# Kernel optimization log

Measured on AMD Instinct MI355X. Metric: run time of the kernel, lower is better.

The kernel has to match this reference:

```python
import jax, jax.numpy as jnp
import numpy as np

B, T, IN, H, OUT, HOR = 512, 720, 6, 128, 3, 360


def _cell(xin, h, c, Wih, Whh, bih, bhh):
    # PyTorch LSTM gate order: i, f, g, o
    g = xin @ Wih.T + h @ Whh.T + bih + bhh
    i, f, gg, o = jnp.split(g, 4, axis=-1)
    c = jax.nn.sigmoid(f) * c + jax.nn.sigmoid(i) * jnp.tanh(gg)
    h = jax.nn.sigmoid(o) * jnp.tanh(c)
    return h, c


def _run_layer(x, Wih, Whh, bih, bhh, reverse):
    xs = x[:, ::-1] if reverse else x
    # hoist input projection out of the scan: (B,T,4H)
    pre = jnp.einsum('bti,gi->btg', xs, Wih) + bih + bhh
    h0 = jnp.zeros((x.shape[0], Whh.shape[1]), x.dtype)

    def step(carry, gt):
        h, c = carry
        g = gt + h @ Whh.T
        i, f, gg, o = jnp.split(g, 4, axis=-1)
        c = jax.nn.sigmoid(f) * c + jax.nn.sigmoid(i) * jnp.tanh(gg)
        h = jax.nn.sigmoid(o) * jnp.tanh(c)
        return (h, c), h

    (hT, cT), ys = jax.lax.scan(step, (h0, h0), jnp.swapaxes(pre, 0, 1))
    ys = jnp.swapaxes(ys, 0, 1)
    if reverse:
        ys = ys[:, ::-1]
    return ys, hT, cT


def reference(x, e0f_Wih, e0f_Whh, e0f_bih, e0f_bhh, e0b_Wih, e0b_Whh, e0b_bih, e0b_bhh,
              e1f_Wih, e1f_Whh, e1f_bih, e1f_bhh, e1b_Wih, e1b_Whh, e1b_bih, e1b_bhh,
              brh_W, brh_b, brc_W, brc_b,
              d0_Wih, d0_Whh, d0_bih, d0_bhh, d1_Wih, d1_Whh, d1_bih, d1_bhh,
              out_W, out_b, start_token):
    b = x.shape[0]
    # bidirectional encoder, layer 0 (input_dim -> H per direction)
    y0f, h0f, c0f = _run_layer(x, e0f_Wih, e0f_Whh, e0f_bih, e0f_bhh, False)
    y0b, h0b, c0b = _run_layer(x, e0b_Wih, e0b_Whh, e0b_bih, e0b_bhh, True)
    y0 = jnp.concatenate([y0f, y0b], axis=-1)  # (B,T,2H)
    # layer 1 (2H -> H per direction); dropout inactive in eval
    _, h1f, c1f = _run_layer(y0, e1f_Wih, e1f_Whh, e1f_bih, e1f_bhh, False)
    _, h1b, c1b = _run_layer(y0, e1b_Wih, e1b_Whh, e1b_bih, e1b_bhh, True)
    # (num_layers, B, 2H): cat fwd/bwd final states per layer
    h_enc = jnp.stack([jnp.concatenate([h0f, h0b], -1), jnp.concatenate([h1f, h1b], -1)])
    c_enc = jnp.stack([jnp.concatenate([c0f, c0b], -1), jnp.concatenate([c1f, c1b], -1)])
    h_dec = h_enc @ brh_W.T + brh_b  # (2,B,H)
    c_dec = c_enc @ brc_W.T + brc_b
    xin0 = jnp.broadcast_to(start_token[0, 0], (b, start_token.shape[-1]))  # (B,3)

    def dec_step(carry, _):
        h0, c0, h1, c1, xin = carry
        h0, c0 = _cell(xin, h0, c0, d0_Wih, d0_Whh, d0_bih, d0_bhh)
        h1, c1 = _cell(h0, h1, c1, d1_Wih, d1_Whh, d1_bih, d1_bhh)
        pred = h1 @ out_W.T + out_b
        return (h0, c0, h1, c1, pred), pred

    carry0 = (h_dec[0], c_dec[0], h_dec[1], c_dec[1], xin0)
    _, preds = jax.lax.scan(dec_step, carry0, None, length=HOR)  # (HOR,B,3)
    return jnp.swapaxes(preds, 0, 1)  # (B,HOR,3)


def setup_inputs() -> dict:
    ks = iter(jax.random.split(jax.random.key(0), 40))

    def p(shape, s=0.05):
        return jax.random.normal(next(ks), shape, dtype=jnp.float32) * s

    d = {"x": jax.random.normal(next(ks), (B, T, IN), dtype=jnp.float32)}
    for name, ind in (("e0f", IN), ("e0b", IN), ("e1f", 2 * H), ("e1b", 2 * H)):
        d[name + "_Wih"] = p((4 * H, ind))
        d[name + "_Whh"] = p((4 * H, H))
        d[name + "_bih"] = p((4 * H,))
        d[name + "_bhh"] = p((4 * H,))
    d["brh_W"] = p((H, 2 * H)); d["brh_b"] = p((H,))
    d["brc_W"] = p((H, 2 * H)); d["brc_b"] = p((H,))
    for name, ind in (("d0", OUT), ("d1", H)):
        d[name + "_Wih"] = p((4 * H, ind))
        d[name + "_Whh"] = p((4 * H, H))
        d[name + "_bih"] = p((4 * H,))
        d[name + "_bhh"] = p((4 * H,))
    d["out_W"] = p((OUT, H)); d["out_b"] = p((OUT,))
    d["start_token"] = p((1, 1, OUT), 0.01)
    return d
```

## Files before the change

kernel.cpp:

```cpp
#include <hip/hip_runtime.h>

typedef __attribute__((ext_vector_type(8))) short bf16x8;
typedef __attribute__((ext_vector_type(4))) float f32x4;

#define MFMA16(a,b,c) __builtin_amdgcn_mfma_f32_16x16x32_bf16((a),(b),(c),0,0,0)

#define T_SEQ  720
#define NB     512
#define HD     128
#define GD     512
#define BT     16
#define HP     136
#define HP0    168
#define YT     256
#define WLP    68
#define HORZ   360

__device__ __forceinline__ float bf2f_(unsigned short u){
  union { unsigned int i; float f; } v; v.i = ((unsigned int)u) << 16; return v.f;
}
__device__ __forceinline__ unsigned short f2bf(float f){
  union { float f; unsigned int i; } v; v.f = f;
  unsigned int r = v.i + 0x7fffu + ((v.i >> 16) & 1u);
  return (unsigned short)(r >> 16);
}
__device__ __forceinline__ float rcp_(float x){ return __builtin_amdgcn_rcpf(x); }
__device__ __forceinline__ float sigm(float x){ return rcp_(1.f + __expf(-x)); }
__device__ __forceinline__ float tanh_(float x){
  float a = fabsf(x);
  float e = __expf(-2.f * a);
  float t = (1.f - e) * rcp_(1.f + e);
  return x >= 0.f ? t : -t;
}
__device__ __forceinline__ bf16x8 cvt8(const float* p){
  bf16x8 r;
  #pragma unroll
  for (int i = 0; i < 8; ++i) r[i] = (short)f2bf(p[i]);
  return r;
}
__device__ __forceinline__ void gl_lds16(const unsigned short* g, unsigned short* l){
  __builtin_amdgcn_global_load_lds(
      (const __attribute__((address_space(1))) void*)(g),
      (__attribute__((address_space(3))) void*)(l), 16, 0, 0);
}

__global__ __launch_bounds__(512, 2)
void enc_layer0_kernel(const float* __restrict__ x,
                       const float* __restrict__ WihF, const float* __restrict__ WhhF,
                       const float* __restrict__ bihF, const float* __restrict__ bhhF,
                       const float* __restrict__ WihB, const float* __restrict__ WhhB,
                       const float* __restrict__ bihB, const float* __restrict__ bhhB,
                       unsigned short* __restrict__ y0,
                       float* __restrict__ ench, float* __restrict__ encc)
{
  __shared__ __align__(16) unsigned short h_buf[2][BT * HP0];
  const int tid  = threadIdx.x;
  const int lane = tid & 63;
  const int w    = tid >> 6;
  const int l15  = lane & 15;
  const int q    = lane >> 4;
  const int dir  = blockIdx.x >> 5;
  const int bbase = (blockIdx.x & 31) * BT;

  const float* Wih = dir ? WihB : WihF;
  const float* Whh = dir ? WhhB : WhhF;
  const float* bih = dir ? bihB : bihF;
  const float* bhh = dir ? bhhB : bhhF;

  bf16x8 bw[4][5];
  float  bias[4];
  #pragma unroll
  for (int g = 0; g < 4; ++g) {
    const int n = g * 128 + w * 16 + l15;
    #pragma unroll
    for (int kt = 0; kt < 4; ++kt)
      bw[g][kt] = cvt8(Whh + n * HD + kt * 32 + q * 8);
    bf16x8 f;
    #pragma unroll
    for (int j = 0; j < 8; ++j) {
      const int kk = q * 8 + j;
      float wv = 0.f;
      if (kk < 6)       wv = Wih[n * 6 + kk];
      else if (kk < 12) wv = Wih[n * 6 + (kk - 6)];
      f[j] = (short)f2bf(wv);
    }
    bw[g][4] = f;
    bias[g] = bih[n] + bhh[n];
  }

  int t = dir ? (T_SEQ - 1) : 0;
  const int dt = dir ? -1 : 1;
  const int xr_ = tid / 6, xk_ = tid % 6;

  float cst[4] = {0.f, 0.f, 0.f, 0.f};
  for (int i = tid; i < 2 * BT * HP0; i += 512) (&h_buf[0][0])[i] = 0;
  __syncthreads();
  float xv_cur = 0.f;
  if (tid < 96) {
    const float v0 = x[((size_t)(bbase + xr_) * T_SEQ + t) * 6 + xk_];
    const unsigned short hi = f2bf(v0);
    h_buf[0][xr_ * HP0 + 128 + xk_] = hi;
    h_buf[0][xr_ * HP0 + 134 + xk_] = f2bf(v0 - bf2f_(hi));
    xv_cur = x[((size_t)(bbase + xr_) * T_SEQ + t + dt) * 6 + xk_];
  }
  __syncthreads();

  for (int s = 0; s < T_SEQ; ++s, t += dt) {
    const int cur = s & 1, nxt = cur ^ 1;

    if (s > 0 && tid < 256) {
      const int b = tid >> 4, c8 = tid & 15;
      const bf16x8 hv = *reinterpret_cast<const bf16x8*>(&h_buf[cur][b * HP0 + c8 * 8]);
      *reinterpret_cast<bf16x8*>(y0 + ((size_t)(bbase + b) * T_SEQ + (t - dt)) * 256 + dir * HD + c8 * 8) = hv;
    }
    float xv_next = 0.f;
    if (tid < 96 && s + 2 < T_SEQ)
      xv_next = x[((size_t)(bbase + xr_) * T_SEQ + (t + 2 * dt)) * 6 + xk_];

    f32x4 acc[4];
    #pragma unroll
    for (int g = 0; g < 4; ++g) {
      acc[g][0] = bias[g]; acc[g][1] = bias[g];
      acc[g][2] = bias[g]; acc[g][3] = bias[g];
    }
    #pragma unroll
    for (int kt = 0; kt < 5; ++kt) {
      const bf16x8 af = *reinterpret_cast<const bf16x8*>(&h_buf[cur][l15 * HP0 + kt * 32 + q * 8]);
      #pragma unroll
      for (int g = 0; g < 4; ++g) acc[g] = MFMA16(af, bw[g][kt], acc[g]);
    }

    #pragma unroll
    for (int r = 0; r < 4; ++r) {
      const float i_ = acc[0][r], f_ = acc[1][r], g_ = acc[2][r], o_ = acc[3][r];
      const float c_ = sigm(f_) * cst[r] + sigm(i_) * tanh_(g_);
      cst[r] = c_;
      const float h_ = sigm(o_) * tanh_(c_);
      h_buf[nxt][(q * 4 + r) * HP0 + w * 16 + l15] = f2bf(h_);
      if (s == T_SEQ - 1) {
        const int b   = bbase + q * 4 + r;
        const int cix = w * 16 + l15;
        ench[(dir * NB + b) * HD + cix] = h_;
        encc[(dir * NB + b) * HD + cix] = c_;
      }
    }
    if (tid < 96 && s + 1 < T_SEQ) {
      const unsigned short hi = f2bf(xv_cur);
      h_buf[nxt][xr_ * HP0 + 128 + xk_] = hi;
      h_buf[nxt][xr_ * HP0 + 134 + xk_] = f2bf(xv_cur - bf2f_(hi));
    }
    xv_cur = xv_next;
    __syncthreads();
  }
  if (tid < 256) {
    const int cur = T_SEQ & 1;
    const int b = tid >> 4, c8 = tid & 15;
    const bf16x8 hv = *reinterpret_cast<const bf16x8*>(&h_buf[cur][b * HP0 + c8 * 8]);
    const int tl = dir ? 0 : (T_SEQ - 1);
    *reinterpret_cast<bf16x8*>(y0 + ((size_t)(bbase + b) * T_SEQ + tl) * 256 + dir * HD + c8 * 8) = hv;
  }
}

__global__ __launch_bounds__(512, 2)
void enc_layer1_kernel(const unsigned short* __restrict__ y0,
                       const float* __restrict__ WihF, const float* __restrict__ WhhF,
                       const float* __restrict__ bihF, const float* __restrict__ bhhF,
                       const float* __restrict__ WihB, const float* __restrict__ WhhB,
                       const float* __restrict__ bihB, const float* __restrict__ bhhB,
                       float* __restrict__ ench, float* __restrict__ encc)
{
  __shared__ __align__(16) unsigned short wlds[GD * WLP];
  __shared__ __align__(16) unsigned short ybuf[2][BT * YT];
  __shared__ __align__(16) unsigned short h_buf[2][BT * HP];

  const int tid  = threadIdx.x;
  const int lane = tid & 63;
  const int w    = tid >> 6;
  const int l15  = lane & 15;
  const int q    = lane >> 4;
  const int dir  = blockIdx.x >> 5;
  const int bbase = (blockIdx.x & 31) * BT;

  const float* Wih = dir ? WihB : WihF;
  const float* Whh = dir ? WhhB : WhhF;
  const float* bih = dir ? bihB : bihF;
  const float* bhh = dir ? bhhB : bhhF;

  for (int i = tid; i < GD * 8; i += 512) {
    const int n = i >> 3, c8 = i & 7;
    *reinterpret_cast<bf16x8*>(&wlds[n * WLP + c8 * 8]) = cvt8(Wih + n * 256 + c8 * 8);
  }

  bf16x8 bw[4][10];
  float  bias[4];
  int    nofs[4];
  #pragma unroll
  for (int g = 0; g < 4; ++g) {
    const int n = g * 128 + w * 16 + l15;
    nofs[g] = n * WLP;
    #pragma unroll
    for (int kt = 2; kt < 8; ++kt)  bw[g][kt - 2] = cvt8(Wih + n * 256 + kt * 32 + q * 8);
    #pragma unroll
    for (int kt = 8; kt < 12; ++kt) bw[g][kt - 2] = cvt8(Whh + n * HD + (kt - 8) * 32 + q * 8);
    bias[g] = bih[n] + bhh[n];
  }

  const int sb   = 2 * w + (lane >> 5);
  const int cimg = lane & 31;
  const int sig  = (cimg & 16) | ((cimg & 15) ^ (sb & 15));
  const size_t grow = (size_t)(bbase + sb) * T_SEQ * 256 + (size_t)sig * 8;
  unsigned short* ldst0 = &ybuf[0][w * 512];
  unsigned short* ldst1 = &ybuf[1][w * 512];

  int t = dir ? (T_SEQ - 1) : 0;
  const int dt = dir ? -1 : 1;

  float cst[4] = {0.f, 0.f, 0.f, 0.f};
  for (int i = tid; i < 2 * BT * HP; i += 512) (&h_buf[0][0])[i] = 0;
  gl_lds16(y0 + grow + (size_t)t * 256, ldst0);
  __syncthreads();

  for (int s = 0; s < T_SEQ; ++s, t += dt) {
    const int cur = s & 1, nxt = cur ^ 1;

    if (s + 1 < T_SEQ)
      gl_lds16(y0 + grow + (size_t)(t + dt) * 256, cur ? ldst0 : ldst1);

    f32x4 acc[4];
    #pragma unroll
    for (int g = 0; g < 4; ++g) {
      acc[g][0] = bias[g]; acc[g][1] = bias[g];
      acc[g][2] = bias[g]; acc[g][3] = bias[g];
    }
    #pragma unroll
    for (int kt = 0; kt < 2; ++kt) {
      const int swz = ((kt * 4 + q) & 15) ^ l15;
      const bf16x8 af = *reinterpret_cast<const bf16x8*>(&ybuf[cur][l15 * YT + swz * 8]);
      #pragma unroll
      for (int g = 0; g < 4; ++g) {
        const bf16x8 bl = *reinterpret_cast<const bf16x8*>(&wlds[nofs[g] + kt * 32 + q * 8]);
        acc[g] = MFMA16(af, bl, acc[g]);
      }
    }
    #pragma unroll
    for (int kt = 2; kt < 8; ++kt) {
      const int c   = kt * 4 + q;
      const int swz = (c & 16) | ((c & 15) ^ l15);
      const bf16x8 af = *reinterpret_cast<const bf16x8*>(&ybuf[cur][l15 * YT + swz * 8]);
      #pragma unroll
      for (int g = 0; g < 4; ++g) acc[g] = MFMA16(af, bw[g][kt - 2], acc[g]);
    }
    #pragma unroll
    for (int kt = 8; kt < 12; ++kt) {
      const bf16x8 af = *reinterpret_cast<const bf16x8*>(&h_buf[cur][l15 * HP + (kt - 8) * 32 + q * 8]);
      #pragma unroll
      for (int g = 0; g < 4; ++g) acc[g] = MFMA16(af, bw[g][kt - 2], acc[g]);
    }

    #pragma unroll
    for (int r = 0; r < 4; ++r) {
      const float i_ = acc[0][r], f_ = acc[1][r], g_ = acc[2][r], o_ = acc[3][r];
      const float c_ = sigm(f_) * cst[r] + sigm(i_) * tanh_(g_);
      cst[r] = c_;
      const float h_ = sigm(o_) * tanh_(c_);
      h_buf[nxt][(q * 4 + r) * HP + w * 16 + l15] = f2bf(h_);
      if (s == T_SEQ - 1) {
        const int b   = bbase + q * 4 + r;
        const int cix = w * 16 + l15;
        ench[(dir * NB + b) * HD + cix] = h_;
        encc[(dir * NB + b) * HD + cix] = c_;
      }
    }
    __syncthreads();
  }
}

__global__ void bridge_kernel(const float* __restrict__ ench0, const float* __restrict__ encc0,
                              const float* __restrict__ ench1, const float* __restrict__ encc1,
                              const float* __restrict__ brhW, const float* __restrict__ brhb,
                              const float* __restrict__ brcW, const float* __restrict__ brcb,
                              float* __restrict__ dech, float* __restrict__ decc)
{
  const int idx = blockIdx.x * 256 + threadIdx.x;
  const int sel = idx >> 17;
  const int l   = (idx >> 16) & 1;
  const int b   = (idx >> 7) & 511;
  const int j   = idx & 127;
  const float* W  = sel ? brcW : brhW;
  const float* bb = sel ? brcb : brhb;
  const float* s0 = sel ? (l ? encc1 : encc0) : (l ? ench1 : ench0);
  float a = bb[j];
  for (int k = 0; k < 128; ++k) a += W[j * 256 + k] * s0[b * 128 + k];
  for (int k = 0; k < 128; ++k) a += W[j * 256 + 128 + k] * s0[(512 + b) * 128 + k];
  float* dst = sel ? decc : dech;
  dst[(l * 512 + b) * 128 + j] = a;
}

__global__ __launch_bounds__(512, 2)
void decoder_kernel(const float* __restrict__ dech, const float* __restrict__ decc,
                    const float* __restrict__ W0ih, const float* __restrict__ W0hh,
                    const float* __restrict__ b0ih, const float* __restrict__ b0hh,
                    const float* __restrict__ W1ih, const float* __restrict__ W1hh,
                    const float* __restrict__ b1ih, const float* __restrict__ b1hh,
                    const float* __restrict__ outW, const float* __restrict__ outb,
                    const float* __restrict__ stok,
                    float* __restrict__ out)
{
  __shared__ __align__(16) unsigned short w0lds[GD * WLP];
  __shared__ __align__(16) unsigned short w1lds[GD * WLP];
  __shared__ __align__(16) unsigned short h0_buf[2][BT * HP];
  __shared__ __align__(16) unsigned short h1_buf[2][BT * HP];

  const int tid  = threadIdx.x;
  const int lane = tid & 63;
  const int w    = tid >> 6;
  const int l15  = lane & 15;
  const int q    = lane >> 4;
  const int bbase = blockIdx.x * BT;

  for (int i = tid; i < GD * 8; i += 512) {
    const int n = i >> 3, c8 = i & 7;
    *reinterpret_cast<bf16x8*>(&w0lds[n * WLP + c8 * 8]) = cvt8(W0hh + n * HD + c8 * 8);
    *reinterpret_cast<bf16x8*>(&w1lds[n * WLP + c8 * 8]) = cvt8(W1ih + n * HD + c8 * 8);
  }

  bf16x8 bw0[4][2];
  bf16x8 bw1[4][6];
  float  xw0[4][3], bias0[4], bias1[4];
  int    nofs[4];
  #pragma unroll
  for (int g = 0; g < 4; ++g) {
    const int n = g * 128 + w * 16 + l15;
    nofs[g] = n * WLP;
    #pragma unroll
    for (int kt = 2; kt < 4; ++kt) {
      bw0[g][kt - 2] = cvt8(W0hh + n * HD + kt * 32 + q * 8);
      bw1[g][kt - 2] = cvt8(W1ih + n * HD + kt * 32 + q * 8);
    }
    #pragma unroll
    for (int kt = 4; kt < 8; ++kt)
      bw1[g][kt - 2] = cvt8(W1hh + n * HD + (kt - 4) * 32 + q * 8);
    #pragma unroll
    for (int k = 0; k < 3; ++k) xw0[g][k] = W0ih[n * 3 + k];
    bias0[g] = b0ih[n] + b0hh[n];
    bias1[g] = b1ih[n] + b1hh[n];
  }

  bf16x8 owf[4];
  float outb_s = 0.f;
  {
    bf16x8 z;
    #pragma unroll
    for (int i = 0; i < 8; ++i) z[i] = 0;
    #pragma unroll
    for (int kt = 0; kt < 4; ++kt) owf[kt] = z;
    if (l15 < 3) {
      #pragma unroll
      for (int kt = 0; kt < 4; ++kt) owf[kt] = cvt8(outW + l15 * HD + kt * 32 + q * 8);
      outb_s = outb[l15];
    }
  }

  float c0[4], c1[4];
  #pragma unroll
  for (int r = 0; r < 4; ++r) {
    const int b   = bbase + q * 4 + r;
    const int cix = w * 16 + l15;
    c0[r] = decc[b * HD + cix];
    c1[r] = decc[(NB + b) * HD + cix];
  }
  for (int i = tid; i < BT * HD; i += 512) {
    const int b = i >> 7, cix = i & 127;
    h0_buf[0][b * HP + cix] = f2bf(dech[(bbase + b) * HD + cix]);
    h1_buf[0][b * HP + cix] = f2bf(dech[(NB + bbase + b) * HD + cix]);
  }
  float xr[4][3];
  {
    const float s0 = stok[0], s1 = stok[1], s2 = stok[2];
    #pragma unroll
    for (int r = 0; r < 4; ++r) { xr[r][0] = s0; xr[r][1] = s1; xr[r][2] = s2; }
  }
  __syncthreads();

  for (int s = 0; s < HORZ; ++s) {
    const int cur = s & 1, nxt = cur ^ 1;

    f32x4 acc[4];
    #pragma unroll
    for (int g = 0; g < 4; ++g)
      #pragma unroll
      for (int r = 0; r < 4; ++r)
        acc[g][r] = bias0[g] + xw0[g][0] * xr[r][0] + xw0[g][1] * xr[r][1] + xw0[g][2] * xr[r][2];
    #pragma unroll
    for (int kt = 0; kt < 2; ++kt) {
      const bf16x8 af = *reinterpret_cast<const bf16x8*>(&h0_buf[cur][l15 * HP + kt * 32 + q * 8]);
      #pragma unroll
      for (int g = 0; g < 4; ++g) {
        const bf16x8 bl = *reinterpret_cast<const bf16x8*>(&w0lds[nofs[g] + kt * 32 + q * 8]);
        acc[g] = MFMA16(af, bl, acc[g]);
      }
    }
    #pragma unroll
    for (int kt = 2; kt < 4; ++kt) {
      const bf16x8 af = *reinterpret_cast<const bf16x8*>(&h0_buf[cur][l15 * HP + kt * 32 + q * 8]);
      #pragma unroll
      for (int g = 0; g < 4; ++g) acc[g] = MFMA16(af, bw0[g][kt - 2], acc[g]);
    }
    #pragma unroll
    for (int r = 0; r < 4; ++r) {
      const float i_ = acc[0][r], f_ = acc[1][r], g_ = acc[2][r], o_ = acc[3][r];
      const float c_ = sigm(f_) * c0[r] + sigm(i_) * tanh_(g_);
      c0[r] = c_;
      const float h_ = sigm(o_) * tanh_(c_);
      h0_buf[nxt][(q * 4 + r) * HP + w * 16 + l15] = f2bf(h_);
    }
    __syncthreads();

    #pragma unroll
    for (int g = 0; g < 4; ++g) {
      acc[g][0] = bias1[g]; acc[g][1] = bias1[g];
      acc[g][2] = bias1[g]; acc[g][3] = bias1[g];
    }
    #pragma unroll
    for (int kt = 0; kt < 2; ++kt) {
      const bf16x8 af = *reinterpret_cast<const bf16x8*>(&h0_buf[nxt][l15 * HP + kt * 32 + q * 8]);
      #pragma unroll
      for (int g = 0; g < 4; ++g) {
        const bf16x8 bl = *reinterpret_cast<const bf16x8*>(&w1lds[nofs[g] + kt * 32 + q * 8]);
        acc[g] = MFMA16(af, bl, acc[g]);
      }
    }
    #pragma unroll
    for (int kt = 2; kt < 4; ++kt) {
      const bf16x8 af = *reinterpret_cast<const bf16x8*>(&h0_buf[nxt][l15 * HP + kt * 32 + q * 8]);
      #pragma unroll
      for (int g = 0; g < 4; ++g) acc[g] = MFMA16(af, bw1[g][kt - 2], acc[g]);
    }
    #pragma unroll
    for (int kt = 4; kt < 8; ++kt) {
      const bf16x8 af = *reinterpret_cast<const bf16x8*>(&h1_buf[cur][l15 * HP + (kt - 4) * 32 + q * 8]);
      #pragma unroll
      for (int g = 0; g < 4; ++g) acc[g] = MFMA16(af, bw1[g][kt - 2], acc[g]);
    }
    #pragma unroll
    for (int r = 0; r < 4; ++r) {
      const float i_ = acc[0][r], f_ = acc[1][r], g_ = acc[2][r], o_ = acc[3][r];
      const float c_ = sigm(f_) * c1[r] + sigm(i_) * tanh_(g_);
      c1[r] = c_;
      const float h_ = sigm(o_) * tanh_(c_);
      h1_buf[nxt][(q * 4 + r) * HP + w * 16 + l15] = f2bf(h_);
    }
    __syncthreads();

    f32x4 p = {0.f, 0.f, 0.f, 0.f};
    #pragma unroll
    for (int kt = 0; kt < 4; ++kt) {
      const bf16x8 af = *reinterpret_cast<const bf16x8*>(&h1_buf[nxt][l15 * HP + kt * 32 + q * 8]);
      p = MFMA16(af, owf[kt], p);
    }
    float pb[4];
    #pragma unroll
    for (int r = 0; r < 4; ++r) pb[r] = p[r] + outb_s;
    if (w == 0 && l15 < 3) {
      #pragma unroll
      for (int r = 0; r < 4; ++r)
        out[((size_t)(bbase + q * 4 + r) * HORZ + s) * 3 + l15] = pb[r];
    }
    #pragma unroll
    for (int r = 0; r < 4; ++r)
      #pragma unroll
      for (int c = 0; c < 3; ++c)
        xr[r][c] = __shfl(pb[r], (q << 4) + c, 64);
  }
}

extern "C" void kernel_launch(void* const* d_in, const int* in_sizes, int n_in,
                              void* d_out, int out_size, void* d_ws, size_t ws_size,
                              hipStream_t stream)
{
  (void)in_sizes; (void)n_in; (void)out_size; (void)ws_size;
  const float* x      = (const float*)d_in[0];
  const float* e0fWih = (const float*)d_in[1];
  const float* e0fWhh = (const float*)d_in[2];
  const float* e0fbih = (const float*)d_in[3];
  const float* e0fbhh = (const float*)d_in[4];
  const float* e0bWih = (const float*)d_in[5];
  const float* e0bWhh = (const float*)d_in[6];
  const float* e0bbih = (const float*)d_in[7];
  const float* e0bbhh = (const float*)d_in[8];
  const float* e1fWih = (const float*)d_in[9];
  const float* e1fWhh = (const float*)d_in[10];
  const float* e1fbih = (const float*)d_in[11];
  const float* e1fbhh = (const float*)d_in[12];
  const float* e1bWih = (const float*)d_in[13];
  const float* e1bWhh = (const float*)d_in[14];
  const float* e1bbih = (const float*)d_in[15];
  const float* e1bbhh = (const float*)d_in[16];
  const float* brhW   = (const float*)d_in[17];
  const float* brhb   = (const float*)d_in[18];
  const float* brcW   = (const float*)d_in[19];
  const float* brcb   = (const float*)d_in[20];
  const float* d0Wih  = (const float*)d_in[21];
  const float* d0Whh  = (const float*)d_in[22];
  const float* d0bih  = (const float*)d_in[23];
  const float* d0bhh  = (const float*)d_in[24];
  const float* d1Wih  = (const float*)d_in[25];
  const float* d1Whh  = (const float*)d_in[26];
  const float* d1bih  = (const float*)d_in[27];
  const float* d1bhh  = (const float*)d_in[28];
  const float* outW   = (const float*)d_in[29];
  const float* outb   = (const float*)d_in[30];
  const float* stok   = (const float*)d_in[31];

  char* ws = (char*)d_ws;
  unsigned short* y0 = (unsigned short*)ws;
  size_t off = (size_t)NB * T_SEQ * 256 * sizeof(unsigned short);
  const size_t blk = (size_t)2 * NB * HD * sizeof(float);
  float* ench0 = (float*)(ws + off); off += blk;
  float* encc0 = (float*)(ws + off); off += blk;
  float* ench1 = (float*)(ws + off); off += blk;
  float* encc1 = (float*)(ws + off); off += blk;
  float* dech  = (float*)(ws + off); off += blk;
  float* decc  = (float*)(ws + off); off += blk;

  enc_layer0_kernel<<<dim3(64), dim3(512), 0, stream>>>(
      x, e0fWih, e0fWhh, e0fbih, e0fbhh, e0bWih, e0bWhh, e0bbih, e0bbhh,
      y0, ench0, encc0);
  enc_layer1_kernel<<<dim3(64), dim3(512), 0, stream>>>(
      y0, e1fWih, e1fWhh, e1fbih, e1fbhh, e1bWih, e1bWhh, e1bbih, e1bbhh,
      ench1, encc1);
  bridge_kernel<<<dim3(1024), dim3(256), 0, stream>>>(
      ench0, encc0, ench1, encc1, brhW, brhb, brcW, brcb, dech, decc);
  decoder_kernel<<<dim3(32), dim3(512), 0, stream>>>(
      dech, decc, d0Wih, d0Whh, d0bih, d0bhh, d1Wih, d1Whh, d1bih, d1bhh,
      outW, outb, stok, (float*)d_out);
}
```

Measured before the change: 3.036 ms.

## Rebalance LDS/register weight split and split MFMA accumulation chains

Moves more of the input-projection weights into LDS (wider padded rows) so fewer weight fragments live in registers in the encoder layer-1 and decoder kernels. The decoder layer-0 weights now live entirely in LDS, while layer-1 weights move fully into registers. The MFMA accumulation is split into two independent chains summed at the end, and the bias is folded in as the first MFMA's accumulator input instead of being written separately. The aim is shorter dependent MFMA chains and less register pressure per step, at the cost of more LDS traffic on the sequential critical path.

After: 3.277 ms. 1.08x slower.

```diff
diff --git a/kernel.cpp b/kernel.cpp
--- a/kernel.cpp
+++ b/kernel.cpp
@@ -13,7 +13,7 @@
 #define HP     136
 #define HP0    168
 #define YT     256
-#define WLP    68
+#define WLP    132
 #define HORZ   360
 
 __device__ __forceinline__ float bf2f_(unsigned short u){
@@ -68,7 +68,7 @@
   const float* bhh = dir ? bhhB : bhhF;
 
   bf16x8 bw[4][5];
-  float  bias[4];
+  f32x4  bias_vec[4];
   #pragma unroll
   for (int g = 0; g < 4; ++g) {
     const int n = g * 128 + w * 16 + l15;
@@ -85,7 +85,8 @@
       f[j] = (short)f2bf(wv);
     }
     bw[g][4] = f;
-    bias[g] = bih[n] + bhh[n];
+    const float b = bih[n] + bhh[n];
+    bias_vec[g][0] = b; bias_vec[g][1] = b; bias_vec[g][2] = b; bias_vec[g][3] = b;
   }
 
   int t = dir ? (T_SEQ - 1) : 0;
@@ -119,15 +120,11 @@
 
     f32x4 acc[4];
     #pragma unroll
-    for (int g = 0; g < 4; ++g) {
-      acc[g][0] = bias[g]; acc[g][1] = bias[g];
-      acc[g][2] = bias[g]; acc[g][3] = bias[g];
-    }
-    #pragma unroll
     for (int kt = 0; kt < 5; ++kt) {
       const bf16x8 af = *reinterpret_cast<const bf16x8*>(&h_buf[cur][l15 * HP0 + kt * 32 + q * 8]);
       #pragma unroll
-      for (int g = 0; g < 4; ++g) acc[g] = MFMA16(af, bw[g][kt], acc[g]);
+      for (int g = 0; g < 4; ++g)
+        acc[g] = MFMA16(af, bw[g][kt], kt == 0 ? bias_vec[g] : acc[g]);
     }
 
     #pragma unroll
@@ -186,23 +183,24 @@
   const float* bih = dir ? bihB : bihF;
   const float* bhh = dir ? bhhB : bhhF;
 
-  for (int i = tid; i < GD * 8; i += 512) {
-    const int n = i >> 3, c8 = i & 7;
+  for (int i = tid; i < GD * 16; i += 512) {
+    const int n = i >> 4, c8 = i & 15;
     *reinterpret_cast<bf16x8*>(&wlds[n * WLP + c8 * 8]) = cvt8(Wih + n * 256 + c8 * 8);
   }
 
-  bf16x8 bw[4][10];
-  float  bias[4];
+  bf16x8 bw[4][8];
+  f32x4  bias_vec[4];
   int    nofs[4];
   #pragma unroll
   for (int g = 0; g < 4; ++g) {
     const int n = g * 128 + w * 16 + l15;
     nofs[g] = n * WLP;
     #pragma unroll
-    for (int kt = 2; kt < 8; ++kt)  bw[g][kt - 2] = cvt8(Wih + n * 256 + kt * 32 + q * 8);
-    #pragma unroll
-    for (int kt = 8; kt < 12; ++kt) bw[g][kt - 2] = cvt8(Whh + n * HD + (kt - 8) * 32 + q * 8);
-    bias[g] = bih[n] + bhh[n];
+    for (int kt = 0; kt < 4; ++kt) bw[g][kt]     = cvt8(Wih + n * 256 + (kt + 4) * 32 + q * 8);
+    #pragma unroll
+    for (int kt = 0; kt < 4; ++kt) bw[g][kt + 4] = cvt8(Whh + n * HD + kt * 32 + q * 8);
+    const float b = bih[n] + bhh[n];
+    bias_vec[g][0] = b; bias_vec[g][1] = b; bias_vec[g][2] = b; bias_vec[g][3] = b;
   }
 
   const int sb   = 2 * w + (lane >> 5);
@@ -226,40 +224,50 @@
     if (s + 1 < T_SEQ)
       gl_lds16(y0 + grow + (size_t)(t + dt) * 256, cur ? ldst0 : ldst1);
 
-    f32x4 acc[4];
-    #pragma unroll
-    for (int g = 0; g < 4; ++g) {
-      acc[g][0] = bias[g]; acc[g][1] = bias[g];
-      acc[g][2] = bias[g]; acc[g][3] = bias[g];
-    }
-    #pragma unroll
-    for (int kt = 0; kt < 2; ++kt) {
-      const int swz = ((kt * 4 + q) & 15) ^ l15;
+    f32x4 accA[4], accB[4];
+    #pragma unroll
+    for (int kt = 0; kt < 4; ++kt) {
+      const int c   = kt * 4 + q;
+      const int swz = (c & 15) ^ l15;
       const bf16x8 af = *reinterpret_cast<const bf16x8*>(&ybuf[cur][l15 * YT + swz * 8]);
       #pragma unroll
       for (int g = 0; g < 4; ++g) {
         const bf16x8 bl = *reinterpret_cast<const bf16x8*>(&wlds[nofs[g] + kt * 32 + q * 8]);
-        acc[g] = MFMA16(af, bl, acc[g]);
+        accA[g] = MFMA16(af, bl, kt == 0 ? bias_vec[g] : accA[g]);
       }
     }
     #pragma unroll
-    for (int kt = 2; kt < 8; ++kt) {
+    for (int kt = 4; kt < 6; ++kt) {
       const int c   = kt * 4 + q;
       const int swz = (c & 16) | ((c & 15) ^ l15);
       const bf16x8 af = *reinterpret_cast<const bf16x8*>(&ybuf[cur][l15 * YT + swz * 8]);
       #pragma unroll
-      for (int g = 0; g < 4; ++g) acc[g] = MFMA16(af, bw[g][kt - 2], acc[g]);
+      for (int g = 0; g < 4; ++g) accA[g] = MFMA16(af, bw[g][kt - 4], accA[g]);
+    }
+    #pragma unroll
+    for (int kt = 6; kt < 8; ++kt) {
+      const int c   = kt * 4 + q;
+      const int swz = (c & 16) | ((c & 15) ^ l15);
+      const bf16x8 af = *reinterpret_cast<const bf16x8*>(&ybuf[cur][l15 * YT + swz * 8]);
+      #pragma unroll
+      for (int g = 0; g < 4; ++g) {
+        const f32x4 z = {0.f, 0.f, 0.f, 0.f};
+        accB[g] = MFMA16(af, bw[g][kt - 4], kt == 6 ? z : accB[g]);
+      }
     }
     #pragma unroll
     for (int kt = 8; kt < 12; ++kt) {
       const bf16x8 af = *reinterpret_cast<const bf16x8*>(&h_buf[cur][l15 * HP + (kt - 8) * 32 + q * 8]);
       #pragma unroll
-      for (int g = 0; g < 4; ++g) acc[g] = MFMA16(af, bw[g][kt - 2], acc[g]);
+      for (int g = 0; g < 4; ++g) accB[g] = MFMA16(af, bw[g][kt - 4], accB[g]);
     }
 
     #pragma unroll
     for (int r = 0; r < 4; ++r) {
-      const float i_ = acc[0][r], f_ = acc[1][r], g_ = acc[2][r], o_ = acc[3][r];
+      const float i_ = accA[0][r] + accB[0][r];
+      const float f_ = accA[1][r] + accB[1][r];
+      const float g_ = accA[2][r] + accB[2][r];
+      const float o_ = accA[3][r] + accB[3][r];
       const float c_ = sigm(f_) * cst[r] + sigm(i_) * tanh_(g_);
       cst[r] = c_;
       const float h_ = sigm(o_) * tanh_(c_);
@@ -307,7 +315,6 @@
                     float* __restrict__ out)
 {
   __shared__ __align__(16) unsigned short w0lds[GD * WLP];
-  __shared__ __align__(16) unsigned short w1lds[GD * WLP];
   __shared__ __align__(16) unsigned short h0_buf[2][BT * HP];
   __shared__ __align__(16) unsigned short h1_buf[2][BT * HP];
 
@@ -318,32 +325,28 @@
   const int q    = lane >> 4;
   const int bbase = blockIdx.x * BT;
 
-  for (int i = tid; i < GD * 8; i += 512) {
-    const int n = i >> 3, c8 = i & 7;
+  for (int i = tid; i < GD * 16; i += 512) {
+    const int n = i >> 4, c8 = i & 15;
     *reinterpret_cast<bf16x8*>(&w0lds[n * WLP + c8 * 8]) = cvt8(W0hh + n * HD + c8 * 8);
-    *reinterpret_cast<bf16x8*>(&w1lds[n * WLP + c8 * 8]) = cvt8(W1ih + n * HD + c8 * 8);
-  }
-
-  bf16x8 bw0[4][2];
-  bf16x8 bw1[4][6];
-  float  xw0[4][3], bias0[4], bias1[4];
+  }
+
+  bf16x8 bw1[4][8];
+  float  xw0[4][3], bias0[4];
+  f32x4  bias1_vec[4];
   int    nofs[4];
   #pragma unroll
   for (int g = 0; g < 4; ++g) {
     const int n = g * 128 + w * 16 + l15;
     nofs[g] = n * WLP;
     #pragma unroll
-    for (int kt = 2; kt < 4; ++kt) {
-      bw0[g][kt - 2] = cvt8(W0hh + n * HD + kt * 32 + q * 8);
-      bw1[g][kt - 2] = cvt8(W1ih + n * HD + kt * 32 + q * 8);
-    }
-    #pragma unroll
-    for (int kt = 4; kt < 8; ++kt)
-      bw1[g][kt - 2] = cvt8(W1hh + n * HD + (kt - 4) * 32 + q * 8);
+    for (int kt = 0; kt < 4; ++kt) bw1[g][kt]     = cvt8(W1ih + n * HD + kt * 32 + q * 8);
+    #pragma unroll
+    for (int kt = 0; kt < 4; ++kt) bw1[g][kt + 4] = cvt8(W1hh + n * HD + kt * 32 + q * 8);
     #pragma unroll
     for (int k = 0; k < 3; ++k) xw0[g][k] = W0ih[n * 3 + k];
     bias0[g] = b0ih[n] + b0hh[n];
-    bias1[g] = b1ih[n] + b1hh[n];
+    const float b1 = b1ih[n] + b1hh[n];
+    bias1_vec[g][0] = b1; bias1_vec[g][1] = b1; bias1_vec[g][2] = b1; bias1_vec[g][3] = b1;
   }
 
   bf16x8 owf[4];
@@ -392,19 +395,13 @@
       for (int r = 0; r < 4; ++r)
         acc[g][r] = bias0[g] + xw0[g][0] * xr[r][0] + xw0[g][1] * xr[r][1] + xw0[g][2] * xr[r][2];
     #pragma unroll
-    for (int kt = 0; kt < 2; ++kt) {
+    for (int kt = 0; kt < 4; ++kt) {
       const bf16x8 af = *reinterpret_cast<const bf16x8*>(&h0_buf[cur][l15 * HP + kt * 32 + q * 8]);
       #pragma unroll
       for (int g = 0; g < 4; ++g) {
         const bf16x8 bl = *reinterpret_cast<const bf16x8*>(&w0lds[nofs[g] + kt * 32 + q * 8]);
         acc[g] = MFMA16(af, bl, acc[g]);
       }
-    }
-    #pragma unroll
-    for (int kt = 2; kt < 4; ++kt) {
-      const bf16x8 af = *reinterpret_cast<const bf16x8*>(&h0_buf[cur][l15 * HP + kt * 32 + q * 8]);
-      #pragma unroll
-      for (int g = 0; g < 4; ++g) acc[g] = MFMA16(af, bw0[g][kt - 2], acc[g]);
     }
     #pragma unroll
     for (int r = 0; r < 4; ++r) {
@@ -416,35 +413,29 @@
     }
     __syncthreads();
 
-    #pragma unroll
-    for (int g = 0; g < 4; ++g) {
-      acc[g][0] = bias1[g]; acc[g][1] = bias1[g];
-      acc[g][2] = bias1[g]; acc[g][3] = bias1[g];
-    }
-    #pragma unroll
-    for (int kt = 0; kt < 2; ++kt) {
+    f32x4 accA[4], accB[4];
+    #pragma unroll
+    for (int kt = 0; kt < 4; ++kt) {
       const bf16x8 af = *reinterpret_cast<const bf16x8*>(&h0_buf[nxt][l15 * HP + kt * 32 + q * 8]);
       #pragma unroll
+      for (int g = 0; g < 4; ++g)
+        accA[g] = MFMA16(af, bw1[g][kt], kt == 0 ? bias1_vec[g] : accA[g]);
+    }
+    #pragma unroll
+    for (int kt = 0; kt < 4; ++kt) {
+      const bf16x8 af = *reinterpret_cast<const bf16x8*>(&h1_buf[cur][l15 * HP + kt * 32 + q * 8]);
+      #pragma unroll
       for (int g = 0; g < 4; ++g) {
-        const bf16x8 bl = *reinterpret_cast<const bf16x8*>(&w1lds[nofs[g] + kt * 32 + q * 8]);
-        acc[g] = MFMA16(af, bl, acc[g]);
+        const f32x4 z = {0.f, 0.f, 0.f, 0.f};
+        accB[g] = MFMA16(af, bw1[g][kt + 4], kt == 0 ? z : accB[g]);
       }
     }
     #pragma unroll
-    for (int kt = 2; kt < 4; ++kt) {
-      const bf16x8 af = *reinterpret_cast<const bf16x8*>(&h0_buf[nxt][l15 * HP + kt * 32 + q * 8]);
-      #pragma unroll
-      for (int g = 0; g < 4; ++g) acc[g] = MFMA16(af, bw1[g][kt - 2], acc[g]);
-    }
-    #pragma unroll
-    for (int kt = 4; kt < 8; ++kt) {
-      const bf16x8 af = *reinterpret_cast<const bf16x8*>(&h1_buf[cur][l15 * HP + (kt - 4) * 32 + q * 8]);
-      #pragma unroll
-      for (int g = 0; g < 4; ++g) acc[g] = MFMA16(af, bw1[g][kt - 2], acc[g]);
-    }
-    #pragma unroll
     for (int r = 0; r < 4; ++r) {
-      const float i_ = acc[0][r], f_ = acc[1][r], g_ = acc[2][r], o_ = acc[3][r];
+      const float i_ = accA[0][r] + accB[0][r];
+      const float f_ = accA[1][r] + accB[1][r];
+      const float g_ = accA[2][r] + accB[2][r];
+      const float o_ = accA[3][r] + accB[3][r];
       const float c_ = sigm(f_) * c1[r] + sigm(i_) * tanh_(g_);
       c1[r] = c_;
       const float h_ = sigm(o_) * tanh_(c_);
```

## Halve encoder block size, give each wave two column tiles in registers

Applied to the files above, without the earlier changes.

Both encoder kernels now launch 256 threads (4 waves) instead of 512. Each wave handles two 16-column tiles per gate, so more of the layer-1 input weights stay in registers and only the first K-chunk is read from LDS, using a narrower LDS pad. The goal is fewer waves taking part in each per-step barrier and less LDS weight traffic on the serial recurrence. The cost is twice as many MFMAs and activations per wave and much higher register pressure (launch bounds of 256,1), which may cause spills or a longer per-step critical path.

Measured after the change: 3.599 ms. +18.5%, slower.

```diff
diff --git a/kernel.cpp b/kernel.cpp
--- a/kernel.cpp
+++ b/kernel.cpp
@@ -13,7 +13,8 @@
 #define HP     136
 #define HP0    168
 #define YT     256
-#define WLP    68
+#define W1LP   36
+#define WDP    68
 #define HORZ   360
 
 __device__ __forceinline__ float bf2f_(unsigned short u){
@@ -44,7 +45,7 @@
       (__attribute__((address_space(3))) void*)(l), 16, 0, 0);
 }
 
-__global__ __launch_bounds__(512, 2)
+__global__ __launch_bounds__(256, 1)
 void enc_layer0_kernel(const float* __restrict__ x,
                        const float* __restrict__ WihF, const float* __restrict__ WhhF,
                        const float* __restrict__ bihF, const float* __restrict__ bhhF,
@@ -67,33 +68,35 @@
   const float* bih = dir ? bihB : bihF;
   const float* bhh = dir ? bhhB : bhhF;
 
-  bf16x8 bw[4][5];
-  float  bias[4];
+  bf16x8 bw[4][2][5];
+  float  bias[4][2];
   #pragma unroll
-  for (int g = 0; g < 4; ++g) {
-    const int n = g * 128 + w * 16 + l15;
-    #pragma unroll
-    for (int kt = 0; kt < 4; ++kt)
-      bw[g][kt] = cvt8(Whh + n * HD + kt * 32 + q * 8);
-    bf16x8 f;
-    #pragma unroll
-    for (int j = 0; j < 8; ++j) {
-      const int kk = q * 8 + j;
-      float wv = 0.f;
-      if (kk < 6)       wv = Wih[n * 6 + kk];
-      else if (kk < 12) wv = Wih[n * 6 + (kk - 6)];
-      f[j] = (short)f2bf(wv);
-    }
-    bw[g][4] = f;
-    bias[g] = bih[n] + bhh[n];
-  }
+  for (int g = 0; g < 4; ++g)
+    #pragma unroll
+    for (int u = 0; u < 2; ++u) {
+      const int n = g * 128 + w * 32 + u * 16 + l15;
+      #pragma unroll
+      for (int kt = 0; kt < 4; ++kt)
+        bw[g][u][kt] = cvt8(Whh + n * HD + kt * 32 + q * 8);
+      bf16x8 f;
+      #pragma unroll
+      for (int j = 0; j < 8; ++j) {
+        const int kk = q * 8 + j;
+        float wv = 0.f;
+        if (kk < 6)       wv = Wih[n * 6 + kk];
+        else if (kk < 12) wv = Wih[n * 6 + (kk - 6)];
+        f[j] = (short)f2bf(wv);
+      }
+      bw[g][u][4] = f;
+      bias[g][u] = bih[n] + bhh[n];
+    }
 
   int t = dir ? (T_SEQ - 1) : 0;
   const int dt = dir ? -1 : 1;
   const int xr_ = tid / 6, xk_ = tid % 6;
 
-  float cst[4] = {0.f, 0.f, 0.f, 0.f};
-  for (int i = tid; i < 2 * BT * HP0; i += 512) (&h_buf[0][0])[i] = 0;
+  float cst[2][4] = {{0.f,0.f,0.f,0.f},{0.f,0.f,0.f,0.f}};
+  for (int i = tid; i < 2 * BT * HP0; i += 256) (&h_buf[0][0])[i] = 0;
   __syncthreads();
   float xv_cur = 0.f;
   if (tid < 96) {
@@ -108,7 +111,7 @@
   for (int s = 0; s < T_SEQ; ++s, t += dt) {
     const int cur = s & 1, nxt = cur ^ 1;
 
-    if (s > 0 && tid < 256) {
+    if (s > 0) {
       const int b = tid >> 4, c8 = tid & 15;
       const bf16x8 hv = *reinterpret_cast<const bf16x8*>(&h_buf[cur][b * HP0 + c8 * 8]);
       *reinterpret_cast<bf16x8*>(y0 + ((size_t)(bbase + b) * T_SEQ + (t - dt)) * 256 + dir * HD + c8 * 8) = hv;
@@ -117,33 +120,40 @@
     if (tid < 96 && s + 2 < T_SEQ)
       xv_next = x[((size_t)(bbase + xr_) * T_SEQ + (t + 2 * dt)) * 6 + xk_];
 
-    f32x4 acc[4];
-    #pragma unroll
-    for (int g = 0; g < 4; ++g) {
-      acc[g][0] = bias[g]; acc[g][1] = bias[g];
-      acc[g][2] = bias[g]; acc[g][3] = bias[g];
-    }
+    f32x4 acc[4][2];
+    #pragma unroll
+    for (int g = 0; g < 4; ++g)
+      #pragma unroll
+      for (int u = 0; u < 2; ++u) {
+        const float b = bias[g][u];
+        acc[g][u][0] = b; acc[g][u][1] = b; acc[g][u][2] = b; acc[g][u][3] = b;
+      }
     #pragma unroll
     for (int kt = 0; kt < 5; ++kt) {
       const bf16x8 af = *reinterpret_cast<const bf16x8*>(&h_buf[cur][l15 * HP0 + kt * 32 + q * 8]);
       #pragma unroll
-      for (int g = 0; g < 4; ++g) acc[g] = MFMA16(af, bw[g][kt], acc[g]);
-    }
-
-    #pragma unroll
-    for (int r = 0; r < 4; ++r) {
-      const float i_ = acc[0][r], f_ = acc[1][r], g_ = acc[2][r], o_ = acc[3][r];
-      const float c_ = sigm(f_) * cst[r] + sigm(i_) * tanh_(g_);
-      cst[r] = c_;
-      const float h_ = sigm(o_) * tanh_(c_);
-      h_buf[nxt][(q * 4 + r) * HP0 + w * 16 + l15] = f2bf(h_);
-      if (s == T_SEQ - 1) {
-        const int b   = bbase + q * 4 + r;
-        const int cix = w * 16 + l15;
-        ench[(dir * NB + b) * HD + cix] = h_;
-        encc[(dir * NB + b) * HD + cix] = c_;
-      }
-    }
+      for (int g = 0; g < 4; ++g)
+        #pragma unroll
+        for (int u = 0; u < 2; ++u)
+          acc[g][u] = MFMA16(af, bw[g][u][kt], acc[g][u]);
+    }
+
+    #pragma unroll
+    for (int u = 0; u < 2; ++u)
+      #pragma unroll
+      for (int r = 0; r < 4; ++r) {
+        const float i_ = acc[0][u][r], f_ = acc[1][u][r], g_ = acc[2][u][r], o_ = acc[3][u][r];
+        const float c_ = sigm(f_) * cst[u][r] + sigm(i_) * tanh_(g_);
+        cst[u][r] = c_;
+        const float h_ = sigm(o_) * tanh_(c_);
+        h_buf[nxt][(q * 4 + r) * HP0 + w * 32 + u * 16 + l15] = f2bf(h_);
+        if (s == T_SEQ - 1) {
+          const int b   = bbase + q * 4 + r;
+          const int cix = w * 32 + u * 16 + l15;
+          ench[(dir * NB + b) * HD + cix] = h_;
+          encc[(dir * NB + b) * HD + cix] = c_;
+        }
+      }
     if (tid < 96 && s + 1 < T_SEQ) {
       const unsigned short hi = f2bf(xv_cur);
       h_buf[nxt][xr_ * HP0 + 128 + xk_] = hi;
@@ -152,7 +162,7 @@
     xv_cur = xv_next;
     __syncthreads();
   }
-  if (tid < 256) {
+  {
     const int cur = T_SEQ & 1;
     const int b = tid >> 4, c8 = tid & 15;
     const bf16x8 hv = *reinterpret_cast<const bf16x8*>(&h_buf[cur][b * HP0 + c8 * 8]);
@@ -161,7 +171,7 @@
   }
 }
 
-__global__ __launch_bounds__(512, 2)
+__global__ __launch_bounds__(256, 1)
 void enc_layer1_kernel(const unsigned short* __restrict__ y0,
                        const float* __restrict__ WihF, const float* __restrict__ WhhF,
                        const float* __restrict__ bihF, const float* __restrict__ bhhF,
@@ -169,7 +179,7 @@
                        const float* __restrict__ bihB, const float* __restrict__ bhhB,
                        float* __restrict__ ench, float* __restrict__ encc)
 {
-  __shared__ __align__(16) unsigned short wlds[GD * WLP];
+  __shared__ __align__(16) unsigned short wlds[GD * W1LP];
   __shared__ __align__(16) unsigned short ybuf[2][BT * YT];
   __shared__ __align__(16) unsigned short h_buf[2][BT * HP];
 
@@ -186,91 +196,114 @@
   const float* bih = dir ? bihB : bihF;
   const float* bhh = dir ? bhhB : bhhF;
 
-  for (int i = tid; i < GD * 8; i += 512) {
-    const int n = i >> 3, c8 = i & 7;
-    *reinterpret_cast<bf16x8*>(&wlds[n * WLP + c8 * 8]) = cvt8(Wih + n * 256 + c8 * 8);
-  }
-
-  bf16x8 bw[4][10];
-  float  bias[4];
-  int    nofs[4];
+  for (int i = tid; i < GD * 4; i += 256) {
+    const int n = i >> 2, c8 = i & 3;
+    *reinterpret_cast<bf16x8*>(&wlds[n * W1LP + c8 * 8]) = cvt8(Wih + n * 256 + c8 * 8);
+  }
+
+  bf16x8 bw[4][2][11];
+  float  bias[4][2];
+  int    nofs[4][2];
   #pragma unroll
-  for (int g = 0; g < 4; ++g) {
-    const int n = g * 128 + w * 16 + l15;
-    nofs[g] = n * WLP;
-    #pragma unroll
-    for (int kt = 2; kt < 8; ++kt)  bw[g][kt - 2] = cvt8(Wih + n * 256 + kt * 32 + q * 8);
-    #pragma unroll
-    for (int kt = 8; kt < 12; ++kt) bw[g][kt - 2] = cvt8(Whh + n * HD + (kt - 8) * 32 + q * 8);
-    bias[g] = bih[n] + bhh[n];
-  }
-
-  const int sb   = 2 * w + (lane >> 5);
+  for (int g = 0; g < 4; ++g)
+    #pragma unroll
+    for (int u = 0; u < 2; ++u) {
+      const int n = g * 128 + w * 32 + u * 16 + l15;
+      nofs[g][u] = n * W1LP;
+      #pragma unroll
+      for (int kt = 1; kt < 8; ++kt)
+        bw[g][u][kt - 1] = cvt8(Wih + n * 256 + kt * 32 + q * 8);
+      #pragma unroll
+      for (int kt = 8; kt < 12; ++kt)
+        bw[g][u][kt - 1] = cvt8(Whh + n * HD + (kt - 8) * 32 + q * 8);
+      bias[g][u] = bih[n] + bhh[n];
+    }
+
+  const int sb0  = 4 * w + (lane >> 5);
+  const int sb1  = sb0 + 2;
   const int cimg = lane & 31;
-  const int sig  = (cimg & 16) | ((cimg & 15) ^ (sb & 15));
-  const size_t grow = (size_t)(bbase + sb) * T_SEQ * 256 + (size_t)sig * 8;
-  unsigned short* ldst0 = &ybuf[0][w * 512];
-  unsigned short* ldst1 = &ybuf[1][w * 512];
+  const int sig0 = (cimg & 16) | ((cimg & 15) ^ (sb0 & 15));
+  const int sig1 = (cimg & 16) | ((cimg & 15) ^ (sb1 & 15));
+  const size_t grow0 = (size_t)(bbase + sb0) * T_SEQ * 256 + (size_t)sig0 * 8;
+  const size_t grow1 = (size_t)(bbase + sb1) * T_SEQ * 256 + (size_t)sig1 * 8;
+  unsigned short* ldA0 = &ybuf[0][(4 * w) * YT];
+  unsigned short* ldA1 = &ybuf[0][(4 * w + 2) * YT];
+  unsigned short* ldB0 = &ybuf[1][(4 * w) * YT];
+  unsigned short* ldB1 = &ybuf[1][(4 * w + 2) * YT];
 
   int t = dir ? (T_SEQ - 1) : 0;
   const int dt = dir ? -1 : 1;
 
-  float cst[4] = {0.f, 0.f, 0.f, 0.f};
-  for (int i = tid; i < 2 * BT * HP; i += 512) (&h_buf[0][0])[i] = 0;
-  gl_lds16(y0 + grow + (size_t)t * 256, ldst0);
+  float cst[2][4] = {{0.f,0.f,0.f,0.f},{0.f,0.f,0.f,0.f}};
+  for (int i = tid; i < 2 * BT * HP; i += 256) (&h_buf[0][0])[i] = 0;
+  gl_lds16(y0 + grow0 + (size_t)t * 256, ldA0);
+  gl_lds16(y0 + grow1 + (size_t)t * 256, ldA1);
   __syncthreads();
 
   for (int s = 0; s < T_SEQ; ++s, t += dt) {
     const int cur = s & 1, nxt = cur ^ 1;
 
-    if (s + 1 < T_SEQ)
-      gl_lds16(y0 + grow + (size_t)(t + dt) * 256, cur ? ldst0 : ldst1);
-
-    f32x4 acc[4];
-    #pragma unroll
-    for (int g = 0; g < 4; ++g) {
-      acc[g][0] = bias[g]; acc[g][1] = bias[g];
-      acc[g][2] = bias[g]; acc[g][3] = bias[g];
-    }
-    #pragma unroll
-    for (int kt = 0; kt < 2; ++kt) {
-      const int swz = ((kt * 4 + q) & 15) ^ l15;
+    if (s + 1 < T_SEQ) {
+      gl_lds16(y0 + grow0 + (size_t)(t + dt) * 256, cur ? ldA0 : ldB0);
+      gl_lds16(y0 + grow1 + (size_t)(t + dt) * 256, cur ? ldA1 : ldB1);
+    }
+
+    f32x4 acc[4][2];
+    #pragma unroll
+    for (int g = 0; g < 4; ++g)
+      #pragma unroll
+      for (int u = 0; u < 2; ++u) {
+        const float b = bias[g][u];
+        acc[g][u][0] = b; acc[g][u][1] = b; acc[g][u][2] = b; acc[g][u][3] = b;
+      }
+    {
+      const int swz = q ^ l15;
       const bf16x8 af = *reinterpret_cast<const bf16x8*>(&ybuf[cur][l15 * YT + swz * 8]);
       #pragma unroll
-      for (int g = 0; g < 4; ++g) {
-        const bf16x8 bl = *reinterpret_cast<const bf16x8*>(&wlds[nofs[g] + kt * 32 + q * 8]);
-        acc[g] = MFMA16(af, bl, acc[g]);
-      }
-    }
-    #pragma unroll
-    for (int kt = 2; kt < 8; ++kt) {
+      for (int g = 0; g < 4; ++g)
+        #pragma unroll
+        for (int u = 0; u < 2; ++u) {
+          const bf16x8 bl = *reinterpret_cast<const bf16x8*>(&wlds[nofs[g][u] + q * 8]);
+          acc[g][u] = MFMA16(af, bl, acc[g][u]);
+        }
+    }
+    #pragma unroll
+    for (int kt = 1; kt < 8; ++kt) {
       const int c   = kt * 4 + q;
       const int swz = (c & 16) | ((c & 15) ^ l15);
       const bf16x8 af = *reinterpret_cast<const bf16x8*>(&ybuf[cur][l15 * YT + swz * 8]);
       #pragma unroll
-      for (int g = 0; g < 4; ++g) acc[g] = MFMA16(af, bw[g][kt - 2], acc[g]);
+      for (int g = 0; g < 4; ++g)
+        #pragma unroll
+        for (int u = 0; u < 2; ++u)
+          acc[g][u] = MFMA16(af, bw[g][u][kt - 1], acc[g][u]);
     }
     #pragma unroll
     for (int kt = 8; kt < 12; ++kt) {
       const bf16x8 af = *reinterpret_cast<const bf16x8*>(&h_buf[cur][l15 * HP + (kt - 8) * 32 + q * 8]);
       #pragma unroll
-      for (int g = 0; g < 4; ++g) acc[g] = MFMA16(af, bw[g][kt - 2], acc[g]);
-    }
-
-    #pragma unroll
-    for (int r = 0; r < 4; ++r) {
-      const float i_ = acc[0][r], f_ = acc[1][r], g_ = acc[2][r], o_ = acc[3][r];
-      const float c_ = sigm(f_) * cst[r] + sigm(i_) * tanh_(g_);
-      cst[r] = c_;
-      const float h_ = sigm(o_) * tanh_(c_);
-      h_buf[nxt][(q * 4 + r) * HP + w * 16 + l15] = f2bf(h_);
-      if (s == T_SEQ - 1) {
-        const int b   = bbase + q * 4 + r;
-        const int cix = w * 16 + l15;
-        ench[(dir * NB + b) * HD + cix] = h_;
-        encc[(dir * NB + b) * HD + cix] = c_;
-      }
-    }
+      for (int g = 0; g < 4; ++g)
+        #pragma unroll
+        for (int u = 0; u < 2; ++u)
+          acc[g][u] = MFMA16(af, bw[g][u][kt - 1], acc[g][u]);
+    }
+
+    #pragma unroll
+    for (int u = 0; u < 2; ++u)
+      #pragma unroll
+      for (int r = 0; r < 4; ++r) {
+        const float i_ = acc[0][u][r], f_ = acc[1][u][r], g_ = acc[2][u][r], o_ = acc[3][u][r];
+        const float c_ = sigm(f_) * cst[u][r] + sigm(i_) * tanh_(g_);
+        cst[u][r] = c_;
+        const float h_ = sigm(o_) * tanh_(c_);
+        h_buf[nxt][(q * 4 + r) * HP + w * 32 + u * 16 + l15] = f2bf(h_);
+        if (s == T_SEQ - 1) {
+          const int b   = bbase + q * 4 + r;
+          const int cix = w * 32 + u * 16 + l15;
+          ench[(dir * NB + b) * HD + cix] = h_;
+          encc[(dir * NB + b) * HD + cix] = c_;
+        }
+      }
     __syncthreads();
   }
 }
@@ -306,8 +339,8 @@
                     const float* __restrict__ stok,
                     float* __restrict__ out)
 {
-  __shared__ __align__(16) unsigned short w0lds[GD * WLP];
-  __shared__ __align__(16) unsigned short w1lds[GD * WLP];
+  __shared__ __align__(16) unsigned short w0lds[GD * WDP];
+  __shared__ __align__(16) unsigned short w1lds[GD * WDP];
   __shared__ __align__(16) unsigned short h0_buf[2][BT * HP];
   __shared__ __align__(16) unsigned short h1_buf[2][BT * HP];
 
@@ -320,8 +353,8 @@
 
   for (int i = tid; i < GD * 8; i += 512) {
     const int n = i >> 3, c8 = i & 7;
-    *reinterpret_cast<bf16x8*>(&w0lds[n * WLP + c8 * 8]) = cvt8(W0hh + n * HD + c8 * 8);
-    *reinterpret_cast<bf16x8*>(&w1lds[n * WLP + c8 * 8]) = cvt8(W1ih + n * HD + c8 * 8);
+    *reinterpret_cast<bf16x8*>(&w0lds[n * WDP + c8 * 8]) = cvt8(W0hh + n * HD + c8 * 8);
+    *reinterpret_cast<bf16x8*>(&w1lds[n * WDP + c8 * 8]) = cvt8(W1ih + n * HD + c8 * 8);
   }
 
   bf16x8 bw0[4][2];
@@ -331,7 +364,7 @@
   #pragma unroll
   for (int g = 0; g < 4; ++g) {
     const int n = g * 128 + w * 16 + l15;
-    nofs[g] = n * WLP;
+    nofs[g] = n * WDP;
     #pragma unroll
     for (int kt = 2; kt < 4; ++kt) {
       bw0[g][kt - 2] = cvt8(W0hh + n * HD + kt * 32 + q * 8);
@@ -523,10 +556,10 @@
   float* dech  = (float*)(ws + off); off += blk;
   float* decc  = (float*)(ws + off); off += blk;
 
-  enc_layer0_kernel<<<dim3(64), dim3(512), 0, stream>>>(
+  enc_layer0_kernel<<<dim3(64), dim3(256), 0, stream>>>(
       x, e0fWih, e0fWhh, e0fbih, e0fbhh, e0bWih, e0bWhh, e0bbih, e0bbhh,
       y0, ench0, encc0);
-  enc_layer1_kernel<<<dim3(64), dim3(512), 0, stream>>>(
+  enc_layer1_kernel<<<dim3(64), dim3(256), 0, stream>>>(
       y0, e1fWih, e1fWhh, e1fbih, e1fbhh, e1bWih, e1bWhh, e1bbih, e1bbhh,
       ench1, encc1);
   bridge_kernel<<<dim3(1024), dim3(256), 0, stream>>>(
```
